# Performance work log

Measured on AMD Instinct MI355X. Metric: run time of the kernel, lower is better.

## Reference

```python
import jax, jax.numpy as jnp
import numpy as np

GAMMA = 0.5
BATCH, DIM, UNITS = 16384, 512, 1024


def setup_inputs() -> dict:
    key = jax.random.key(0)
    k1, k2 = jax.random.split(key)
    inputs = jax.random.normal(k1, (BATCH, DIM), dtype=jnp.float32)
    mu = jax.random.normal(k2, (DIM, UNITS), dtype=jnp.float32)
    return {"inputs": inputs, "mu": mu}


def reference(inputs, mu):
    # Squared L2 distance from each input row to each center (column of mu):
    x_sq = jnp.sum(inputs * inputs, axis=1, keepdims=True)        # [B, 1]
    mu_sq = jnp.sum(mu * mu, axis=0, keepdims=True)               # [1, U]
    cross = inputs @ mu                                           # [B, U] GEMM
    l2 = x_sq - 2.0 * cross + mu_sq                                # [B, U]
    return jnp.exp(-GAMMA * l2)
```

## Files before the change

### kernel.cpp

```cpp
#include <hip/hip_runtime.h>

#define BATCH 16384
#define DIM   512
#define UNITS 1024

typedef float v16f __attribute__((ext_vector_type(16)));
#define MFMA_F8(a, b, c) __builtin_amdgcn_mfma_f32_32x32x16_fp8_fp8((a), (b), (c), 0, 0, 0)

__device__ __forceinline__ int2 cvt8(const float4 f0, const float4 f1) {
    int lo = __builtin_amdgcn_cvt_pk_fp8_f32(f0.x, f0.y, 0, false);
    lo     = __builtin_amdgcn_cvt_pk_fp8_f32(f0.z, f0.w, lo, true);
    int hi = __builtin_amdgcn_cvt_pk_fp8_f32(f1.x, f1.y, 0, false);
    hi     = __builtin_amdgcn_cvt_pk_fp8_f32(f1.z, f1.w, hi, true);
    return make_int2(lo, hi);
}
__device__ __forceinline__ float dot8(const float4 f0, const float4 f1) {
    return f0.x * f0.x + f0.y * f0.y + f0.z * f0.z + f0.w * f0.w
         + f1.x * f1.x + f1.y * f1.y + f1.z * f1.z + f1.w * f1.w;
}

__global__ __launch_bounds__(512, 4)
void rbf_fused_kernel(const float* __restrict__ in, const float* __restrict__ mu,
                      float* __restrict__ out) {
    __shared__ __attribute__((aligned(16))) unsigned char smem[75264];
    unsigned char* Bs = smem;
    unsigned char* As = smem + 65536;
    float* musq_red = (float*)(smem + 73728);
    float* musq_l   = (float*)(smem + 74752);
    float* xsq_red  = (float*)smem;
    float* xsq_l    = (float*)(smem + 2048);

    const int t  = threadIdx.x;
    const int l  = t & 63;
    const int w  = t >> 6;
    const int ln = l & 31;
    const int h  = l >> 5;

    const int b   = blockIdx.x;
    const int xcd = b & 7;
    const int j   = b >> 3;
    const int m0  = (xcd * 8 + (j & 7)) * 256;
    const int n0  = (j >> 3) * 128;
    const int wm  = (w >> 1) * 64;
    const int wn  = (w & 1) * 64;

    const int ar = t >> 1, seg = t & 1;
    const float* arow = in + (size_t)(m0 + ar) * DIM + seg * 8;
    const int aidx = (((ar >> 5) * 64) + seg * 32 + (ar & 31)) * 8;

    float4 ga[2][2];
    ga[0][0] = ((const float4*)arow)[0];
    ga[0][1] = ((const float4*)arow)[1];
    ga[1][0] = ((const float4*)(arow + 16))[0];
    ga[1][1] = ((const float4*)(arow + 16))[1];

    {
        const int ng  = w >> 1;
        const int kwb = (w & 1) * 16;
        const float* msrc = mu + (size_t)(kwb * 16 + h * 8) * UNITS + n0 + ng * 32 + ln;
        unsigned char* bdst = Bs + (((ng * 32 + kwb) * 64) + l) * 8;
        float s = 0.f;
#pragma unroll 4
        for (int kk = 0; kk < 16; kk++) {
            float v[8];
#pragma unroll
            for (int jj = 0; jj < 8; jj++) v[jj] = msrc[(size_t)(kk * 16 + jj) * UNITS];
#pragma unroll
            for (int jj = 0; jj < 8; jj++) s += v[jj] * v[jj];
            int lo = __builtin_amdgcn_cvt_pk_fp8_f32(v[0], v[1], 0, false);
            lo     = __builtin_amdgcn_cvt_pk_fp8_f32(v[2], v[3], lo, true);
            int hi = __builtin_amdgcn_cvt_pk_fp8_f32(v[4], v[5], 0, false);
            hi     = __builtin_amdgcn_cvt_pk_fp8_f32(v[6], v[7], hi, true);
            *(int2*)(bdst + kk * 512) = make_int2(lo, hi);
        }
        s += __shfl_xor(s, 32, 64);
        if (h == 0) musq_red[(ng * 32 + ln) * 2 + (w & 1)] = s;
    }

    float sA = dot8(ga[0][0], ga[0][1]);
    *(int2*)(As + aidx) = cvt8(ga[0][0], ga[0][1]);
    __syncthreads();
    if (t < 128) musq_l[t] = -0.5f * (musq_red[t * 2] + musq_red[t * 2 + 1]);

    const long* BsL = (const long*)Bs;
    v16f acc[2][2];
#pragma unroll
    for (int c = 0; c < 2; c++)
#pragma unroll
        for (int g = 0; g < 2; g++) acc[c][g] = (v16f)0.f;

#pragma unroll 2
    for (int i = 0; i < 32; i++) {
        if (i < 30) {
            ga[i & 1][0] = ((const float4*)(arow + (i + 2) * 16))[0];
            ga[i & 1][1] = ((const float4*)(arow + (i + 2) * 16))[1];
        }
        const long* AsL = (const long*)(As + (i & 1) * 4096);
        long a0 = AsL[((w >> 1) * 2 + 0) * 64 + l];
        long a1 = AsL[((w >> 1) * 2 + 1) * 64 + l];
        long b0 = BsL[(((w & 1) * 2 + 0) * 32 + i) * 64 + l];
        long b1 = BsL[(((w & 1) * 2 + 1) * 32 + i) * 64 + l];
        acc[0][0] = MFMA_F8(a0, b0, acc[0][0]);
        acc[0][1] = MFMA_F8(a0, b1, acc[0][1]);
        acc[1][0] = MFMA_F8(a1, b0, acc[1][0]);
        acc[1][1] = MFMA_F8(a1, b1, acc[1][1]);
        if (i < 31) {
            sA += dot8(ga[(i + 1) & 1][0], ga[(i + 1) & 1][1]);
            *(int2*)(As + ((i + 1) & 1) * 4096 + aidx)
                = cvt8(ga[(i + 1) & 1][0], ga[(i + 1) & 1][1]);
        }
        __syncthreads();
    }

    xsq_red[ar * 2 + seg] = sA;
    __syncthreads();
    if (t < 256)
        xsq_l[t] = -0.5f * (xsq_red[t * 2] + xsq_red[t * 2 + 1]);
    __syncthreads();

#pragma unroll
    for (int c = 0; c < 2; c++) {
        const size_t mrow = m0 + wm + c * 32;
#pragma unroll
        for (int g = 0; g < 2; g++) {
            const int nc = n0 + wn + g * 32;
            const float mb = musq_l[wn + g * 32 + ln];
#pragma unroll
            for (int r = 0; r < 16; r++) {
                const int rl = (r & 3) + 8 * (r >> 2) + 4 * h;
                const float xb = xsq_l[wm + c * 32 + rl];
                float v = __expf(acc[c][g][r] + xb + mb);
                __builtin_nontemporal_store(
                    v, out + (mrow + rl) * UNITS + nc + ln);
            }
        }
    }
}

extern "C" void kernel_launch(void* const* d_in, const int* in_sizes, int n_in,
                              void* d_out, int out_size, void* d_ws, size_t ws_size,
                              hipStream_t stream) {
    const float* inputs = (const float*)d_in[0];
    const float* mu     = (const float*)d_in[1];
    float* out = (float*)d_out;
    (void)d_ws; (void)ws_size;

    rbf_fused_kernel<<<512, 512, 0, stream>>>(inputs, mu, out);
}
```

Measured before the change: 122.6 us.

## Load A fragments directly into registers per wave, removing shared A staging and barriers

Each wave now owns a 32-row strip of the 256-row tile and all 128 columns. It loads its own input rows from global memory straight into MFMA operand registers, converting to fp8 on the fly. This removes the shared-memory A buffer and the per-iteration __syncthreads, and row norms are now reduced with a cross-lane shuffle instead of through shared memory. In exchange, every K step needs four B loads from LDS per wave, B traffic per wave doubles, and each wave's global load pattern for A becomes strided across rows.

```diff
diff --git a/kernel.cpp b/kernel.cpp
--- a/kernel.cpp
+++ b/kernel.cpp
@@ -7,14 +7,14 @@
 typedef float v16f __attribute__((ext_vector_type(16)));
 #define MFMA_F8(a, b, c) __builtin_amdgcn_mfma_f32_32x32x16_fp8_fp8((a), (b), (c), 0, 0, 0)
 
-__device__ __forceinline__ int2 cvt8(const float4 f0, const float4 f1) {
+static __device__ __forceinline__ long cvt8(const float4 f0, const float4 f1) {
     int lo = __builtin_amdgcn_cvt_pk_fp8_f32(f0.x, f0.y, 0, false);
     lo     = __builtin_amdgcn_cvt_pk_fp8_f32(f0.z, f0.w, lo, true);
     int hi = __builtin_amdgcn_cvt_pk_fp8_f32(f1.x, f1.y, 0, false);
     hi     = __builtin_amdgcn_cvt_pk_fp8_f32(f1.z, f1.w, hi, true);
-    return make_int2(lo, hi);
+    return (long)(unsigned)lo | ((long)hi << 32);
 }
-__device__ __forceinline__ float dot8(const float4 f0, const float4 f1) {
+static __device__ __forceinline__ float dot8(const float4 f0, const float4 f1) {
     return f0.x * f0.x + f0.y * f0.y + f0.z * f0.z + f0.w * f0.w
          + f1.x * f1.x + f1.y * f1.y + f1.z * f1.z + f1.w * f1.w;
 }
@@ -22,13 +22,10 @@
 __global__ __launch_bounds__(512, 4)
 void rbf_fused_kernel(const float* __restrict__ in, const float* __restrict__ mu,
                       float* __restrict__ out) {
-    __shared__ __attribute__((aligned(16))) unsigned char smem[75264];
+    __shared__ __attribute__((aligned(16))) unsigned char smem[67072];
     unsigned char* Bs = smem;
-    unsigned char* As = smem + 65536;
-    float* musq_red = (float*)(smem + 73728);
-    float* musq_l   = (float*)(smem + 74752);
-    float* xsq_red  = (float*)smem;
-    float* xsq_l    = (float*)(smem + 2048);
+    float* musq_red = (float*)(smem + 65536);
+    float* musq_l   = (float*)(smem + 66560);
 
     const int t  = threadIdx.x;
     const int l  = t & 63;
@@ -41,24 +38,16 @@
     const int j   = b >> 3;
     const int m0  = (xcd * 8 + (j & 7)) * 256;
     const int n0  = (j >> 3) * 128;
-    const int wm  = (w >> 1) * 64;
-    const int wn  = (w & 1) * 64;
 
-    const int ar = t >> 1, seg = t & 1;
-    const float* arow = in + (size_t)(m0 + ar) * DIM + seg * 8;
-    const int aidx = (((ar >> 5) * 64) + seg * 32 + (ar & 31)) * 8;
-
-    float4 ga[2][2];
-    ga[0][0] = ((const float4*)arow)[0];
-    ga[0][1] = ((const float4*)arow)[1];
-    ga[1][0] = ((const float4*)(arow + 16))[0];
-    ga[1][1] = ((const float4*)(arow + 16))[1];
+    const float4* ap = (const float4*)(in + (size_t)(m0 + w * 32 + ln) * DIM + h * 8);
+    float4 p0a = ap[0], p0b = ap[1];
+    float4 p1a = ap[4], p1b = ap[5];
 
     {
-        const int ng  = w >> 1;
-        const int kwb = (w & 1) * 16;
-        const float* msrc = mu + (size_t)(kwb * 16 + h * 8) * UNITS + n0 + ng * 32 + ln;
-        unsigned char* bdst = Bs + (((ng * 32 + kwb) * 64) + l) * 8;
+        const int ng = w >> 1;
+        const int kq = w & 1;
+        const float* msrc = mu + (size_t)(kq * 256 + h * 8) * UNITS + n0 + ng * 32 + ln;
+        unsigned char* bdst = Bs + (size_t)(((ng * 32 + kq * 16) * 64) + l) * 8;
         float s = 0.f;
 #pragma unroll 4
         for (int kk = 0; kk < 16; kk++) {
@@ -67,73 +56,61 @@
             for (int jj = 0; jj < 8; jj++) v[jj] = msrc[(size_t)(kk * 16 + jj) * UNITS];
 #pragma unroll
             for (int jj = 0; jj < 8; jj++) s += v[jj] * v[jj];
-            int lo = __builtin_amdgcn_cvt_pk_fp8_f32(v[0], v[1], 0, false);
-            lo     = __builtin_amdgcn_cvt_pk_fp8_f32(v[2], v[3], lo, true);
-            int hi = __builtin_amdgcn_cvt_pk_fp8_f32(v[4], v[5], 0, false);
-            hi     = __builtin_amdgcn_cvt_pk_fp8_f32(v[6], v[7], hi, true);
-            *(int2*)(bdst + kk * 512) = make_int2(lo, hi);
+            *(long*)(bdst + kk * 512) =
+                cvt8(make_float4(v[0], v[1], v[2], v[3]),
+                     make_float4(v[4], v[5], v[6], v[7]));
         }
         s += __shfl_xor(s, 32, 64);
-        if (h == 0) musq_red[(ng * 32 + ln) * 2 + (w & 1)] = s;
+        if (h == 0) musq_red[(ng * 32 + ln) * 2 + kq] = s;
     }
-
-    float sA = dot8(ga[0][0], ga[0][1]);
-    *(int2*)(As + aidx) = cvt8(ga[0][0], ga[0][1]);
     __syncthreads();
     if (t < 128) musq_l[t] = -0.5f * (musq_red[t * 2] + musq_red[t * 2 + 1]);
+    __syncthreads();
 
     const long* BsL = (const long*)Bs;
-    v16f acc[2][2];
-#pragma unroll
-    for (int c = 0; c < 2; c++)
-#pragma unroll
-        for (int g = 0; g < 2; g++) acc[c][g] = (v16f)0.f;
+    v16f acc0 = (v16f)0.f, acc1 = (v16f)0.f, acc2 = (v16f)0.f, acc3 = (v16f)0.f;
+    float sA = 0.f;
 
 #pragma unroll 2
     for (int i = 0; i < 32; i++) {
+        const float4 f0 = (i & 1) ? p1a : p0a;
+        const float4 f1 = (i & 1) ? p1b : p0b;
+        sA += dot8(f0, f1);
+        const long a = cvt8(f0, f1);
         if (i < 30) {
-            ga[i & 1][0] = ((const float4*)(arow + (i + 2) * 16))[0];
-            ga[i & 1][1] = ((const float4*)(arow + (i + 2) * 16))[1];
+            if (i & 1) { p1a = ap[(i + 2) * 4]; p1b = ap[(i + 2) * 4 + 1]; }
+            else       { p0a = ap[(i + 2) * 4]; p0b = ap[(i + 2) * 4 + 1]; }
         }
-        const long* AsL = (const long*)(As + (i & 1) * 4096);
-        long a0 = AsL[((w >> 1) * 2 + 0) * 64 + l];
-        long a1 = AsL[((w >> 1) * 2 + 1) * 64 + l];
-        long b0 = BsL[(((w & 1) * 2 + 0) * 32 + i) * 64 + l];
-        long b1 = BsL[(((w & 1) * 2 + 1) * 32 + i) * 64 + l];
-        acc[0][0] = MFMA_F8(a0, b0, acc[0][0]);
-        acc[0][1] = MFMA_F8(a0, b1, acc[0][1]);
-        acc[1][0] = MFMA_F8(a1, b0, acc[1][0]);
-        acc[1][1] = MFMA_F8(a1, b1, acc[1][1]);
-        if (i < 31) {
-            sA += dot8(ga[(i + 1) & 1][0], ga[(i + 1) & 1][1]);
-            *(int2*)(As + ((i + 1) & 1) * 4096 + aidx)
-                = cvt8(ga[(i + 1) & 1][0], ga[(i + 1) & 1][1]);
-        }
-        __syncthreads();
+        const int bo = i * 64 + l;
+        const long b0 = BsL[bo];
+        const long b1 = BsL[bo + 2048];
+        const long b2 = BsL[bo + 4096];
+        const long b3 = BsL[bo + 6144];
+        acc0 = MFMA_F8(a, b0, acc0);
+        acc1 = MFMA_F8(a, b1, acc1);
+        acc2 = MFMA_F8(a, b2, acc2);
+        acc3 = MFMA_F8(a, b3, acc3);
     }
 
-    xsq_red[ar * 2 + seg] = sA;
-    __syncthreads();
-    if (t < 256)
-        xsq_l[t] = -0.5f * (xsq_red[t * 2] + xsq_red[t * 2 + 1]);
-    __syncthreads();
+    sA += __shfl_xor(sA, 32, 64);
+    const float xv = -0.5f * sA;
 
+    const float mb0 = musq_l[ln];
+    const float mb1 = musq_l[32 + ln];
+    const float mb2 = musq_l[64 + ln];
+    const float mb3 = musq_l[96 + ln];
+
+    const size_t mrow = m0 + w * 32;
+    float* obase = out + n0 + ln;
 #pragma unroll
-    for (int c = 0; c < 2; c++) {
-        const size_t mrow = m0 + wm + c * 32;
-#pragma unroll
-        for (int g = 0; g < 2; g++) {
-            const int nc = n0 + wn + g * 32;
-            const float mb = musq_l[wn + g * 32 + ln];
-#pragma unroll
-            for (int r = 0; r < 16; r++) {
-                const int rl = (r & 3) + 8 * (r >> 2) + 4 * h;
-                const float xb = xsq_l[wm + c * 32 + rl];
-                float v = __expf(acc[c][g][r] + xb + mb);
-                __builtin_nontemporal_store(
-                    v, out + (mrow + rl) * UNITS + nc + ln);
-            }
-        }
+    for (int r = 0; r < 16; r++) {
+        const int rl = (r & 3) + 8 * (r >> 2) + 4 * h;
+        const float xb = __shfl(xv, rl, 64);
+        float* orow = obase + (mrow + rl) * UNITS;
+        __builtin_nontemporal_store(__expf(acc0[r] + xb + mb0), orow);
+        __builtin_nontemporal_store(__expf(acc1[r] + xb + mb1), orow + 32);
+        __builtin_nontemporal_store(__expf(acc2[r] + xb + mb2), orow + 64);
+        __builtin_nontemporal_store(__expf(acc3[r] + xb + mb3), orow + 96);
     }
 }
 
```

Measured after the change: 128.0 us. +4.4%, slower.
